# Kernel tuning notes

Measured on AMD Instinct MI355X. Metric: run time of the kernel, lower is better.

## Reference

```python
import jax, jax.numpy as jnp
import numpy as np

B, S, D_IN, D_OUT = 4, 2048, 1024, 1024
N_TREES, DEPTH, N_HEADS = 12, 3, 3
N_INTERNAL = 2 ** DEPTH - 1  # 7
N_LEAVES = 2 ** DEPTH        # 8
TEMPERATURE = 1.0
SOFTPLUS_SHIFT = 0.5413      # softplus(0.5413) ~= 1.0, so init node temp ~ 1


def _build_path_indices(depth):
    """Root-to-leaf internal-node indices and go-left directions per leaf."""
    L = 2 ** depth
    pi = np.zeros((L, depth), np.int32)
    pd = np.zeros((L, depth), np.float32)
    for leaf in range(L):
        node = 0
        for d in range(depth):
            pi[leaf, d] = node
            bit = (leaf >> (depth - 1 - d)) & 1
            pd[leaf, d] = 1.0 - bit
            node = 2 * node + 1 + bit
    return pi, pd


def setup_inputs() -> dict:
    key = jax.random.key(0)
    ks = jax.random.split(key, 4)
    x = jax.random.normal(ks[0], (B, S, D_IN), dtype=jnp.float32)
    # normal(0, 0.1) routing init
    decision_weights = 0.1 * jax.random.normal(ks[1], (N_TREES, N_INTERNAL, D_IN), dtype=jnp.float32)
    decision_biases = jnp.zeros((N_TREES, N_INTERNAL), dtype=jnp.float32)
    node_temperature_logits = jnp.zeros((N_TREES, N_INTERNAL), dtype=jnp.float32)
    # nn.Linear default init ~ U(-1/sqrt(D), 1/sqrt(D)); use matching-scale normal
    gate_w = jax.random.normal(ks[2], (N_TREES, D_IN), dtype=jnp.float32) / np.sqrt(D_IN)
    gate_b = jnp.zeros((N_TREES,), dtype=jnp.float32)
    # xavier_normal over each [n_leaves, output_dim] slice
    xav_std = np.sqrt(2.0 / (N_LEAVES + D_OUT))
    leaf_outputs = xav_std * jax.random.normal(ks[3], (N_HEADS, N_TREES, N_LEAVES, D_OUT), dtype=jnp.float32)
    pi, pd = _build_path_indices(DEPTH)
    return {
        "x": x,
        "decision_weights": decision_weights,
        "decision_biases": decision_biases,
        "node_temperature_logits": node_temperature_logits,
        "gate_w": gate_w,
        "gate_b": gate_b,
        "leaf_outputs": leaf_outputs,
        "path_indices": jnp.asarray(pi),
        "path_dirs": jnp.asarray(pd),
    }


def reference(x, decision_weights, decision_biases, node_temperature_logits,
              gate_w, gate_b, leaf_outputs, path_indices, path_dirs):
    # decisions: [B, S, T, N_internal]
    decisions = jnp.einsum('bsd,tnd->bstn', x, decision_weights) + decision_biases
    node_temps = TEMPERATURE * jax.nn.softplus(node_temperature_logits + SOFTPLUS_SHIFT)
    decisions = jax.nn.sigmoid(decisions / node_temps)
    # gather nodes along each root->leaf path: [B, S, T, L, depth]
    relevant = decisions[..., path_indices]
    probs_per_level = path_dirs * relevant + (1.0 - path_dirs) * (1.0 - relevant)
    leaf_probs = probs_per_level.prod(axis=-1)  # [B, S, T, L]
    # softmax gate over trees: [B, S, T]
    weights = jax.nn.softmax(jnp.einsum('bsd,td->bst', x, gate_w) + gate_b, axis=-1)
    # fold tree gate into leaf probs, then contract leaves against leaf outputs
    routed = leaf_probs * weights[..., None]            # [B, S, T, L]
    out = jnp.einsum('bstl,htld->hbsd', routed, leaf_outputs)  # [H, B, S, Dout]
    return out
```

## Files before the change

### kernel.cpp

```cpp
#include <hip/hip_runtime.h>

typedef __attribute__((ext_vector_type(8))) short short8;
typedef __attribute__((ext_vector_type(4))) float floatx4;
typedef unsigned int uint;
typedef unsigned short ushort;
typedef __attribute__((ext_vector_type(4))) uint uintx4;

#define NTOK   8192
#define DIN    1024
#define DOUT   1024
#define NJ     96
#define TOKPB  32
#define XSTR   136
#define DSTR   97
#define SSTR   85
#define LOT_H  (DOUT * NJ)

static __device__ inline ushort f2b(float f) {
    uint u = __builtin_bit_cast(uint, f);
    u = u + 0x7fffu + ((u >> 16) & 1u);
    return (ushort)(u >> 16);
}
static __device__ inline uint pack2(float a, float b) {
    return (uint)f2b(a) | ((uint)f2b(b) << 16);
}

__global__ __launch_bounds__(256) void k_prep(const float* __restrict__ lo,
                                              const float* __restrict__ dw,
                                              const float* __restrict__ gw,
                                              ushort* __restrict__ lot,
                                              ushort* __restrict__ wcat) {
    int i = blockIdx.x * 256 + threadIdx.x;
    if (i < 3 * LOT_H) {
        int h = i / LOT_H;
        int rem = i - h * LOT_H;
        int k = rem >> 10;
        int d = rem & 1023;
        lot[h * LOT_H + d * NJ + k] = f2b(lo[i]);
    } else {
        int j = i - 3 * LOT_H;
        int r = j >> 10, c = j & 1023;
        float v = (r < 84) ? dw[r * DIN + c] : gw[(r - 84) * DIN + c];
        wcat[j] = f2b(v);
    }
}

__global__ __launch_bounds__(256) void k_routed(
    const float* __restrict__ x,
    const ushort* __restrict__ wcat,
    const float* __restrict__ db,
    const float* __restrict__ ntl,
    const float* __restrict__ gb,
    const int*   __restrict__ pi,
    const float* __restrict__ pd,
    ushort* __restrict__ routed)
{
    __shared__ __attribute__((aligned(16))) char smem[34816];
    __shared__ float invt[84];
    __shared__ float biasf[96];
    __shared__ int   pis[24];
    __shared__ float pds[24];

    ushort* xl = (ushort*)smem;
    ushort* wl = (ushort*)(smem + TOKPB * XSTR * 2);
    float*  decis = (float*)smem;
    float*  sdecs = (float*)(smem + TOKPB * DSTR * 4);

    const int tid = threadIdx.x;
    const int tb  = blockIdx.x * TOKPB;

    if (tid < 84) {
        float z = ntl[tid] + 0.5413f;
        float sp = (z > 20.0f) ? z : log1pf(__expf(z));
        invt[tid]  = 1.0f / sp;
        biasf[tid] = db[tid];
    } else if (tid < 96) {
        biasf[tid] = gb[tid - 84];
    } else if (tid < 120) {
        pis[tid - 96] = pi[tid - 96];
    } else if (tid < 144) {
        pds[tid - 120] = pd[tid - 120];
    }

    const int wave = tid >> 6, lane = tid & 63;
    const int lrow = lane & 15, quad = lane >> 4;
    const int wm = wave & 1, wn = wave >> 1;

    floatx4 acc[3];
#pragma unroll
    for (int nt = 0; nt < 3; ++nt) acc[nt] = (floatx4)(0.0f);

    for (int kc = 0; kc < 8; ++kc) {
        __syncthreads();
#pragma unroll
        for (int i = 0; i < 4; ++i) {
            int idx = tid + 256 * i;
            int r = idx >> 5, c = idx & 31;
            float4 v = *(const float4*)(x + (size_t)(tb + r) * DIN + kc * 128 + c * 4);
            uint2 p;
            p.x = pack2(v.x, v.y);
            p.y = pack2(v.z, v.w);
            *(uint2*)(xl + r * XSTR + c * 4) = p;
        }
#pragma unroll
        for (int i = 0; i < 6; ++i) {
            int idx = tid + 256 * i;
            int r = idx >> 4, c = idx & 15;
            uintx4 v = *(const uintx4*)(wcat + r * DIN + kc * 128 + c * 8);
            *(uintx4*)(wl + r * XSTR + c * 8) = v;
        }
        __syncthreads();

        short8 a[4];
#pragma unroll
        for (int kt = 0; kt < 4; ++kt)
            a[kt] = *(const short8*)(xl + (wm * 16 + lrow) * XSTR + kt * 32 + quad * 8);
#pragma unroll
        for (int nt = 0; nt < 3; ++nt) {
#pragma unroll
            for (int kt = 0; kt < 4; ++kt) {
                short8 b = *(const short8*)(wl + (wn * 48 + nt * 16 + lrow) * XSTR + kt * 32 + quad * 8);
                acc[nt] = __builtin_amdgcn_mfma_f32_16x16x32_bf16(a[kt], b, acc[nt], 0, 0, 0);
            }
        }
    }

    __syncthreads();
#pragma unroll
    for (int nt = 0; nt < 3; ++nt)
#pragma unroll
        for (int r = 0; r < 4; ++r)
            decis[(wm * 16 + quad * 4 + r) * DSTR + wn * 48 + nt * 16 + lrow] = acc[nt][r];
    __syncthreads();

#pragma unroll
    for (int i = 0; i < 11; ++i) {
        int idx = tid + 256 * i;
        if (idx < TOKPB * 84) {
            int tk = idx / 84, nd = idx - tk * 84;
            float dv = (decis[tk * DSTR + nd] + biasf[nd]) * invt[nd];
            sdecs[tk * SSTR + nd] = 1.0f / (1.0f + __expf(-dv));
        }
    }
    __syncthreads();

    {
        const int tk = tid >> 3, l = tid & 7;
        float g[12], gm = -1e30f;
#pragma unroll
        for (int tt = 0; tt < 12; ++tt) {
            g[tt] = decis[tk * DSTR + 84 + tt] + biasf[84 + tt];
            gm = fmaxf(gm, g[tt]);
        }
        float gs = 0.0f;
#pragma unroll
        for (int tt = 0; tt < 12; ++tt) { g[tt] = __expf(g[tt] - gm); gs += g[tt]; }
        float ginv = 1.0f / gs;

        const int   n0 = pis[l * 3 + 0], n1 = pis[l * 3 + 1], n2 = pis[l * 3 + 2];
        const float d0 = pds[l * 3 + 0], d1 = pds[l * 3 + 1], d2 = pds[l * 3 + 2];
        const float* sd = sdecs + tk * SSTR;
        ushort* dst = routed + (size_t)(tb + tk) * NJ + l;
#pragma unroll
        for (int t = 0; t < 12; ++t) {
            float s0 = sd[t * 7 + n0], s1 = sd[t * 7 + n1], s2 = sd[t * 7 + n2];
            float pb = g[t] * ginv
                     * (d0 * s0 + (1.0f - d0) * (1.0f - s0))
                     * (d1 * s1 + (1.0f - d1) * (1.0f - s1))
                     * (d2 * s2 + (1.0f - d2) * (1.0f - s2));
            dst[t * 8] = f2b(pb);
        }
    }
}

__global__ __launch_bounds__(256) void k_out(
    const ushort* __restrict__ routed,
    const ushort* __restrict__ lot,
    float* __restrict__ out)
{
    const int tb = blockIdx.x * 64;
    const int d0 = blockIdx.y * 64;
    const int h  = blockIdx.z;
    const int wave = threadIdx.x >> 6, lane = threadIdx.x & 63;
    const int lrow = lane & 15, quad = lane >> 4;

    const ushort* ap = routed + (size_t)(tb + wave * 16 + lrow) * NJ + quad * 8;
    short8 a[3];
#pragma unroll
    for (int kk = 0; kk < 3; ++kk) a[kk] = *(const short8*)(ap + kk * 32);

    const ushort* bp = lot + (size_t)h * LOT_H + (size_t)(d0 + lrow) * NJ + quad * 8;
    floatx4 acc[4];
#pragma unroll
    for (int nt = 0; nt < 4; ++nt) {
        acc[nt] = (floatx4)(0.0f);
#pragma unroll
        for (int kk = 0; kk < 3; ++kk) {
            short8 b = *(const short8*)(bp + nt * 16 * NJ + kk * 32);
            acc[nt] = __builtin_amdgcn_mfma_f32_16x16x32_bf16(a[kk], b, acc[nt], 0, 0, 0);
        }
    }
#pragma unroll
    for (int nt = 0; nt < 4; ++nt) {
        int d = d0 + nt * 16 + lrow;
#pragma unroll
        for (int r = 0; r < 4; ++r) {
            int tok = tb + wave * 16 + quad * 4 + r;
            out[((size_t)h * NTOK + tok) * DOUT + d] = acc[nt][r];
        }
    }
}

extern "C" void kernel_launch(void* const* d_in, const int* in_sizes, int n_in,
                              void* d_out, int out_size, void* d_ws, size_t ws_size,
                              hipStream_t stream) {
    const float* x   = (const float*)d_in[0];
    const float* dw  = (const float*)d_in[1];
    const float* db  = (const float*)d_in[2];
    const float* ntl = (const float*)d_in[3];
    const float* gw  = (const float*)d_in[4];
    const float* gb  = (const float*)d_in[5];
    const float* lo  = (const float*)d_in[6];
    const int*   pi  = (const int*)d_in[7];
    const float* pd  = (const float*)d_in[8];
    float* out = (float*)d_out;

    ushort* routed = (ushort*)d_ws;
    ushort* lot    = routed + (size_t)NTOK * NJ;
    ushort* wcat   = lot + (size_t)3 * LOT_H;

    k_prep<<<dim3((3 * LOT_H + NJ * DIN) / 256), dim3(256), 0, stream>>>(lo, dw, gw, lot, wcat);
    k_routed<<<dim3(NTOK / TOKPB), dim3(256), 0, stream>>>(x, wcat, db, ntl, gb, pi, pd, routed);
    k_out<<<dim3(NTOK / 64, DOUT / 64, 3), dim3(256), 0, stream>>>(routed, lot, out);
}
```

Baseline: 166.3 us.

## Vectorize prep transposes, prefetch x in routed GEMM, stage tiles in LDS for output

The prep kernel now writes transposed leaf outputs and concatenated weights with 16-byte vector stores, each thread converting eight elements. This cuts the grid to 192 blocks. The routed kernel register-prefetches the next 128-column chunk of x while the current chunk runs on MFMA, which hides global load latency. The output kernel stages the routed and leaf tiles into padded shared memory with coalesced vector loads instead of strided per-lane global reads. This costs extra LDS and a barrier.

```diff
diff --git a/kernel.cpp b/kernel.cpp
--- a/kernel.cpp
+++ b/kernel.cpp
@@ -14,6 +14,7 @@
 #define XSTR   136
 #define DSTR   97
 #define SSTR   85
+#define OSTR   104
 #define LOT_H  (DOUT * NJ)
 
 static __device__ inline ushort f2b(float f) {
@@ -31,17 +32,27 @@
                                               ushort* __restrict__ lot,
                                               ushort* __restrict__ wcat) {
     int i = blockIdx.x * 256 + threadIdx.x;
-    if (i < 3 * LOT_H) {
-        int h = i / LOT_H;
-        int rem = i - h * LOT_H;
-        int k = rem >> 10;
-        int d = rem & 1023;
-        lot[h * LOT_H + d * NJ + k] = f2b(lo[i]);
+    if (i < 36864) {
+        int h   = i / 12288;
+        int rem = i - h * 12288;
+        int d   = rem / 12;
+        int kg  = rem - d * 12;
+        const float* src = lo + (size_t)h * LOT_H + (size_t)kg * 8 * DOUT + d;
+        ushort tmp[8];
+#pragma unroll
+        for (int j = 0; j < 8; ++j) tmp[j] = f2b(src[j * DOUT]);
+        *(uintx4*)(lot + (size_t)h * LOT_H + d * NJ + kg * 8) = *(uintx4*)tmp;
     } else {
-        int j = i - 3 * LOT_H;
-        int r = j >> 10, c = j & 1023;
-        float v = (r < 84) ? dw[r * DIN + c] : gw[(r - 84) * DIN + c];
-        wcat[j] = f2b(v);
+        int j = i - 36864;
+        int r = j >> 7, cg = j & 127;
+        const float* src = (r < 84) ? (dw + (size_t)r * DIN) : (gw + (size_t)(r - 84) * DIN);
+        src += cg * 8;
+        float4 v0 = *(const float4*)(src);
+        float4 v1 = *(const float4*)(src + 4);
+        uintx4 p;
+        p.x = pack2(v0.x, v0.y); p.y = pack2(v0.z, v0.w);
+        p.z = pack2(v1.x, v1.y); p.w = pack2(v1.z, v1.w);
+        *(uintx4*)(wcat + (size_t)r * DIN + cg * 8) = p;
     }
 }
 
@@ -86,30 +97,39 @@
     const int lrow = lane & 15, quad = lane >> 4;
     const int wm = wave & 1, wn = wave >> 1;
 
+    const int xr = tid >> 5, xc = tid & 31;
+
     floatx4 acc[3];
 #pragma unroll
     for (int nt = 0; nt < 3; ++nt) acc[nt] = (floatx4)(0.0f);
+
+    float4 xp[4];
+#pragma unroll
+    for (int i = 0; i < 4; ++i)
+        xp[i] = *(const float4*)(x + (size_t)(tb + xr + i * 8) * DIN + xc * 4);
 
     for (int kc = 0; kc < 8; ++kc) {
         __syncthreads();
 #pragma unroll
         for (int i = 0; i < 4; ++i) {
-            int idx = tid + 256 * i;
-            int r = idx >> 5, c = idx & 31;
-            float4 v = *(const float4*)(x + (size_t)(tb + r) * DIN + kc * 128 + c * 4);
             uint2 p;
-            p.x = pack2(v.x, v.y);
-            p.y = pack2(v.z, v.w);
-            *(uint2*)(xl + r * XSTR + c * 4) = p;
+            p.x = pack2(xp[i].x, xp[i].y);
+            p.y = pack2(xp[i].z, xp[i].w);
+            *(uint2*)(xl + (xr + i * 8) * XSTR + xc * 4) = p;
         }
 #pragma unroll
         for (int i = 0; i < 6; ++i) {
             int idx = tid + 256 * i;
             int r = idx >> 4, c = idx & 15;
-            uintx4 v = *(const uintx4*)(wcat + r * DIN + kc * 128 + c * 8);
+            uintx4 v = *(const uintx4*)(wcat + (size_t)r * DIN + kc * 128 + c * 8);
             *(uintx4*)(wl + r * XSTR + c * 8) = v;
         }
         __syncthreads();
+        if (kc < 7) {
+#pragma unroll
+            for (int i = 0; i < 4; ++i)
+                xp[i] = *(const float4*)(x + (size_t)(tb + xr + i * 8) * DIN + (kc + 1) * 128 + xc * 4);
+        }
 
         short8 a[4];
 #pragma unroll
@@ -178,25 +198,42 @@
     const ushort* __restrict__ lot,
     float* __restrict__ out)
 {
+    __shared__ __attribute__((aligned(16))) ushort al[64 * OSTR];
+    __shared__ __attribute__((aligned(16))) ushort bl[64 * OSTR];
+
+    const int tid = threadIdx.x;
     const int tb = blockIdx.x * 64;
     const int d0 = blockIdx.y * 64;
     const int h  = blockIdx.z;
-    const int wave = threadIdx.x >> 6, lane = threadIdx.x & 63;
+
+    const ushort* asrc = routed + (size_t)tb * NJ;
+    const ushort* bsrc = lot + ((size_t)h * DOUT + d0) * NJ;
+#pragma unroll
+    for (int i = 0; i < 3; ++i) {
+        int flat = tid + i * 256;
+        int row = flat / 12, col = (flat % 12) * 8;
+        uintx4 va = *(const uintx4*)(asrc + flat * 8);
+        *(uintx4*)(al + row * OSTR + col) = va;
+        uintx4 vb = *(const uintx4*)(bsrc + flat * 8);
+        *(uintx4*)(bl + row * OSTR + col) = vb;
+    }
+    __syncthreads();
+
+    const int wave = tid >> 6, lane = tid & 63;
     const int lrow = lane & 15, quad = lane >> 4;
 
-    const ushort* ap = routed + (size_t)(tb + wave * 16 + lrow) * NJ + quad * 8;
     short8 a[3];
 #pragma unroll
-    for (int kk = 0; kk < 3; ++kk) a[kk] = *(const short8*)(ap + kk * 32);
-
-    const ushort* bp = lot + (size_t)h * LOT_H + (size_t)(d0 + lrow) * NJ + quad * 8;
+    for (int kk = 0; kk < 3; ++kk)
+        a[kk] = *(const short8*)(al + (wave * 16 + lrow) * OSTR + kk * 32 + quad * 8);
+
     floatx4 acc[4];
 #pragma unroll
     for (int nt = 0; nt < 4; ++nt) {
         acc[nt] = (floatx4)(0.0f);
 #pragma unroll
         for (int kk = 0; kk < 3; ++kk) {
-            short8 b = *(const short8*)(bp + nt * 16 * NJ + kk * 32);
+            short8 b = *(const short8*)(bl + (nt * 16 + lrow) * OSTR + kk * 32 + quad * 8);
             acc[nt] = __builtin_amdgcn_mfma_f32_16x16x32_bf16(a[kk], b, acc[nt], 0, 0, 0);
         }
     }
@@ -229,7 +266,7 @@
     ushort* lot    = routed + (size_t)NTOK * NJ;
     ushort* wcat   = lot + (size_t)3 * LOT_H;
 
-    k_prep<<<dim3((3 * LOT_H + NJ * DIN) / 256), dim3(256), 0, stream>>>(lo, dw, gw, lot, wcat);
+    k_prep<<<dim3(192), dim3(256), 0, stream>>>(lo, dw, gw, lot, wcat);
     k_routed<<<dim3(NTOK / TOKPB), dim3(256), 0, stream>>>(x, wcat, db, ntl, gb, pi, pd, routed);
     k_out<<<dim3(NTOK / 64, DOUT / 64, 3), dim3(256), 0, stream>>>(routed, lot, out);
 }
```

Result: no change. 167.4 us (+0.7%).
